# Optimization experiments

Measured on AMD Instinct MI355X. Metric: run time of the kernel, lower is better.

The kernel has to match this reference:

```python
import jax, jax.numpy as jnp
import numpy as np

B, H, W, C = 32, 64, 64, 512
NUM_HEADS = 16
WS = 8          # window_size
SHIFT = 4       # shift_size = WS // 2
MLP_HIDDEN = 2048
N = WS * WS     # tokens per window
NW = (H // WS) * (W // WS)  # windows per image


def _rel_coords_table():
    # Swin-V2 log-spaced continuous relative coordinates, (1, 2*WS-1, 2*WS-1, 2)
    r = np.arange(-(WS - 1), WS, dtype=np.float32)
    t = np.stack(np.meshgrid(r, r, indexing='ij'), axis=-1)[None]
    t = t / (WS - 1) * 8.0
    t = np.sign(t) * np.log2(np.abs(t) + 1.0) / np.log2(8.0)
    return t.astype(np.float32)


def _rel_pos_index():
    coords = np.stack(np.meshgrid(np.arange(WS), np.arange(WS), indexing='ij'))
    cf = coords.reshape(2, -1)
    rel = (cf[:, :, None] - cf[:, None, :]).transpose(1, 2, 0)
    rel[..., 0] += WS - 1
    rel[..., 1] += WS - 1
    rel[..., 0] *= 2 * WS - 1
    return rel.sum(-1)  # (N, N) int


def _attn_mask():
    # shifted-window mask: -100 where tokens come from different image regions
    img = np.zeros((H, W), np.float32)
    cnt = 0
    for hs in (slice(0, -WS), slice(-WS, -SHIFT), slice(-SHIFT, None)):
        for ws_ in (slice(0, -WS), slice(-WS, -SHIFT), slice(-SHIFT, None)):
            img[hs, ws_] = cnt
            cnt += 1
    mw = img.reshape(H // WS, WS, W // WS, WS).transpose(0, 2, 1, 3).reshape(-1, N)
    diff = mw[:, None, :] - mw[:, :, None]
    return np.where(diff != 0, np.float32(-100.0), np.float32(0.0))  # (NW, N, N)


_RCT = jnp.asarray(_rel_coords_table())
_RPI = jnp.asarray(_rel_pos_index().reshape(-1))
_MASK = jnp.asarray(_attn_mask())
_LOGIT_MAX = float(np.log(1.0 / 0.01))


def _layernorm(x, w, b):
    mu = x.mean(-1, keepdims=True)
    var = ((x - mu) ** 2).mean(-1, keepdims=True)
    return (x - mu) / jnp.sqrt(var + 1e-5) * w + b


def setup_inputs() -> dict:
    key = jax.random.key(0)
    ks = jax.random.split(key, 8)
    s = 0.02
    return {
        'x': jax.random.normal(ks[0], (B, H * W, C), jnp.float32),
        'qkv_w': jax.random.normal(ks[1], (3 * C, C), jnp.float32) * s,
        'q_bias': jnp.zeros((C,), jnp.float32),
        'v_bias': jnp.zeros((C,), jnp.float32),
        'logit_scale': jnp.log(10.0 * jnp.ones((NUM_HEADS, 1, 1), jnp.float32)),
        'cpb_w1': jax.random.normal(ks[2], (512, 2), jnp.float32) * s,
        'cpb_b1': jnp.zeros((512,), jnp.float32),
        'cpb_w2': jax.random.normal(ks[3], (NUM_HEADS, 512), jnp.float32) * s,
        'proj_w': jax.random.normal(ks[4], (C, C), jnp.float32) * s,
        'proj_b': jnp.zeros((C,), jnp.float32),
        'norm1_w': jnp.ones((C,), jnp.float32),
        'norm1_b': jnp.zeros((C,), jnp.float32),
        'norm2_w': jnp.ones((C,), jnp.float32),
        'norm2_b': jnp.zeros((C,), jnp.float32),
        'fc1_w': jax.random.normal(ks[5], (MLP_HIDDEN, C), jnp.float32) * s,
        'fc1_b': jnp.zeros((MLP_HIDDEN,), jnp.float32),
        'fc2_w': jax.random.normal(ks[6], (C, MLP_HIDDEN), jnp.float32) * s,
        'fc2_b': jnp.zeros((C,), jnp.float32),
    }


def reference(x, qkv_w, q_bias, v_bias, logit_scale, cpb_w1, cpb_b1, cpb_w2,
              proj_w, proj_b, norm1_w, norm1_b, norm2_w, norm2_b,
              fc1_w, fc1_b, fc2_w, fc2_b):
    hd = C // NUM_HEADS
    shortcut = x
    xi = x.reshape(B, H, W, C)
    xi = jnp.roll(xi, shift=(-SHIFT, -SHIFT), axis=(1, 2))
    # window partition -> (B*NW, N, C)
    xw = xi.reshape(B, H // WS, WS, W // WS, WS, C).transpose(0, 1, 3, 2, 4, 5).reshape(-1, N, C)
    # qkv with q/v bias only (k bias = 0), Swin-V2 style
    qkv_b = jnp.concatenate([q_bias, jnp.zeros_like(v_bias), v_bias])
    qkv = (xw @ qkv_w.T + qkv_b).reshape(-1, N, 3, NUM_HEADS, hd).transpose(2, 0, 3, 1, 4)
    q, k, v = qkv[0], qkv[1], qkv[2]  # (B_, nH, N, hd)
    # cosine attention
    qn = q / jnp.maximum(jnp.linalg.norm(q, axis=-1, keepdims=True), 1e-12)
    kn = k / jnp.maximum(jnp.linalg.norm(k, axis=-1, keepdims=True), 1e-12)
    attn = jnp.einsum('whnd,whmd->whnm', qn, kn)
    scale = jnp.exp(jnp.minimum(logit_scale, _LOGIT_MAX))  # (nH,1,1)
    attn = attn * scale
    # continuous relative position bias via small MLP
    table = (jax.nn.relu(_RCT @ cpb_w1.T + cpb_b1) @ cpb_w2.T).reshape(-1, NUM_HEADS)
    bias = table[_RPI].reshape(N, N, NUM_HEADS).transpose(2, 0, 1)  # (nH, N, N)
    bias = 16.0 * jax.nn.sigmoid(bias)
    attn = attn + bias[None]
    # shift mask
    attn = attn.reshape(B, NW, NUM_HEADS, N, N) + _MASK[None, :, None]
    attn = jax.nn.softmax(attn.reshape(-1, NUM_HEADS, N, N), axis=-1)
    out = jnp.einsum('whnm,whmd->whnd', attn, v).transpose(0, 2, 1, 3).reshape(-1, N, C)
    out = out @ proj_w.T + proj_b
    # window reverse + un-shift
    xi = out.reshape(B, H // WS, W // WS, WS, WS, C).transpose(0, 1, 3, 2, 4, 5).reshape(B, H, W, C)
    xi = jnp.roll(xi, shift=(SHIFT, SHIFT), axis=(1, 2)).reshape(B, H * W, C)
    # Swin-V2 post-norm residuals
    x = shortcut + _layernorm(xi, norm1_w, norm1_b)
    h = jax.nn.gelu(x @ fc1_w.T + fc1_b, approximate=False)
    y = h @ fc2_w.T + fc2_b
    x = x + _layernorm(y, norm2_w, norm2_b)
    return x
```

## Files before the change

kernel.cpp:

```cpp
#include <hip/hip_runtime.h>

typedef unsigned short u16;
typedef unsigned int u32;
typedef __attribute__((ext_vector_type(8))) __bf16 bf16x8;
typedef __attribute__((ext_vector_type(8))) short s16x8;
typedef __attribute__((ext_vector_type(4))) short s16x4;
typedef __attribute__((ext_vector_type(4))) float f32x4;

static __device__ __forceinline__ float bf2f(u16 h){
  union{u32 u; float f;} v; v.u = ((u32)h)<<16; return v.f;
}
static __device__ __forceinline__ u16 cvtbf(float f){
  return __builtin_bit_cast(u16, (__bf16)f);
}

#define GLD16(gp, lp) __builtin_amdgcn_global_load_lds(                      \
  (__attribute__((address_space(1))) void*)(void*)(gp),                      \
  (__attribute__((address_space(3))) void*)(void*)(lp), 16, 0, 0)

__global__ __launch_bounds__(256)
void prep_x_kernel(const float* __restrict__ x, u16* __restrict__ xw)
{
  const int t = threadIdx.x, wv = t>>6, ln = t&63;
  const size_t row = (size_t)blockIdx.x*4 + wv;
  const int b = (int)(row>>12), wl = (int)((row>>6)&63), m = (int)(row&63);
  const int gh = ((wl>>3)*8 + (m>>3) + 4) & 63;
  const int gw = ((wl&7)*8 + (m&7) + 4) & 63;
  const size_t src = ((size_t)b*4096 + (size_t)gh*64 + gw)*512 + (size_t)ln*8;
  f32x4 a = *(const f32x4*)&x[src];
  f32x4 c = *(const f32x4*)&x[src+4];
  s16x8 o;
#pragma unroll
  for (int j=0;j<4;j++){ o[j] = (short)cvtbf(a[j]); o[j+4] = (short)cvtbf(c[j]); }
  *(s16x8*)&xw[row*512 + (size_t)ln*8] = o;
}

__global__ __launch_bounds__(256)
void cvt_bf16_kernel(const float* __restrict__ src, u16* __restrict__ dst, int n)
{
  const int i = (blockIdx.x*256 + threadIdx.x)*8;
  if (i >= n) return;
  f32x4 a = *(const f32x4*)&src[i];
  f32x4 c = *(const f32x4*)&src[i+4];
  s16x8 o;
#pragma unroll
  for (int j=0;j<4;j++){ o[j] = (short)cvtbf(a[j]); o[j+4] = (short)cvtbf(c[j]); }
  *(s16x8*)&dst[i] = o;
}

static __device__ __forceinline__ float logcoord(int d){
  const float tt = (float)d * (8.0f/7.0f);
  const float sg = (tt > 0.f) ? 1.f : ((tt < 0.f) ? -1.f : 0.f);
  return sg * log2f(fabsf(tt) + 1.f) * (1.f/3.f);
}

__global__ __launch_bounds__(512)
void cpb_table_kernel(const float* __restrict__ w1, const float* __restrict__ b1,
                      const float* __restrict__ w2, float* __restrict__ table)
{
  __shared__ float hid[512];
  const int r = blockIdx.x, j = threadIdx.x;
  const float va = logcoord(r/15 - 7);
  const float vb = logcoord(r%15 - 7);
  hid[j] = fmaxf(va*w1[2*j] + vb*w1[2*j+1] + b1[j], 0.f);
  __syncthreads();
  if (j < 16){
    float acc = 0.f;
    for (int i=0;i<512;i++) acc += hid[i]*w2[j*512+i];
    table[r*16 + j] = acc;
  }
}

__global__ __launch_bounds__(256)
void bias_expand_kernel(const float* __restrict__ table, float* __restrict__ biasT)
{
  const int gid = blockIdx.x*256 + threadIdx.x;
  const int h = gid>>12, ij = gid&4095, i = ij>>6, j = ij&63;
  const int dr = (i>>3)-(j>>3)+7, dc = (i&7)-(j&7)+7;
  const float v = table[(dr*15+dc)*16 + h];
  biasT[gid] = 16.f / (1.f + __expf(-v));
}

template<int EPI>
__global__ __launch_bounds__(512)
void gemm256(const u16* __restrict__ A, const u16* __restrict__ B,
             u16* __restrict__ Co, const float* __restrict__ bias0,
             const float* __restrict__ bias1, int N, int K)
{
  extern __shared__ u16 ls[];
  const int t = threadIdx.x;
  const int wv = t>>6, ln = t&63;
  const int wr = wv>>2, wc = wv&3;
  const int lr = ln&15, lg = ln>>4;
  const int gx = gridDim.x;
  const int lin = blockIdx.y*gx + blockIdx.x;
  const int q = (gx*(int)gridDim.y)>>3;
  const int lin2 = (lin&7)*q + (lin>>3);
  const int mT = lin2/gx, nT = lin2 - mT*gx;

  const int rS = wv*32 + (ln>>2);
  const int cS = ((ln&3) ^ ((ln>>3)&3)) * 8;
  const u16* gA0 = A + (size_t)(mT*256 + rS)*K + cS;
  const u16* gB0 = B + (size_t)(nT*256 + rS)*K + cS;
  const size_t rstep = (size_t)16*K;
  char* lW = (char*)ls + wv*2048;

  const int cR = (lg ^ ((lr>>1)&3))*8;
  const int offA0 = (wr*128 + lr)*32 + cR;
  const int offB0 = (wc*64  + lr)*32 + cR;

#define STAGE(buf, tt) do {                                                  \
    char* lb_ = lW + (buf)*32768;                                            \
    const size_t ko_ = (size_t)(tt)*32;                                      \
    GLD16(gA0 + ko_,         lb_);                                           \
    GLD16(gA0 + ko_ + rstep, lb_ + 1024);                                    \
    GLD16(gB0 + ko_,         lb_ + 16384);                                   \
    GLD16(gB0 + ko_ + rstep, lb_ + 16384 + 1024);                            \
  } while(0)

  f32x4 acc[8][4] = {};

#define COMPUTE(buf) do {                                                    \
    const u16* la_ = ls + (buf)*16384;                                       \
    const u16* lb2_ = la_ + 8192;                                            \
    bf16x8 bfr[4];                                                           \
    _Pragma("unroll")                                                        \
    for (int nt=0;nt<4;nt++) bfr[nt] = *(const bf16x8*)&lb2_[offB0 + nt*512];\
    __builtin_amdgcn_s_setprio(1);                                           \
    _Pragma("unroll")                                                        \
    for (int mt=0;mt<8;mt++){                                                \
      bf16x8 af = *(const bf16x8*)&la_[offA0 + mt*512];                      \
      _Pragma("unroll")                                                      \
      for (int nt=0;nt<4;nt++)                                               \
        acc[mt][nt] = __builtin_amdgcn_mfma_f32_16x16x32_bf16(af, bfr[nt], acc[mt][nt], 0,0,0); \
    }                                                                        \
    __builtin_amdgcn_s_setprio(0);                                           \
  } while(0)

  const int nsteps = K>>5;
  STAGE(0,0); STAGE(1,1); STAGE(2,2);
  int cb = 0, sb = 3;
  for (int t_=3; t_<nsteps; ++t_){
    STAGE(sb, t_); sb = (sb==4)?0:sb+1;
    asm volatile("s_waitcnt vmcnt(12)\n\ts_barrier" ::: "memory");
    COMPUTE(cb); cb = (cb==4)?0:cb+1;
  }
  asm volatile("s_waitcnt vmcnt(8)\n\ts_barrier" ::: "memory");
  COMPUTE(cb); cb = (cb==4)?0:cb+1;
  asm volatile("s_waitcnt vmcnt(4)\n\ts_barrier" ::: "memory");
  COMPUTE(cb); cb = (cb==4)?0:cb+1;
  asm volatile("s_waitcnt vmcnt(0)\n\ts_barrier" ::: "memory");
  COMPUTE(cb);
#undef STAGE
#undef COMPUTE

  if (EPI == 0) {
    const int cb0 = nT*256 + wc*64;
    int secA[4], hhA[4], dA[4]; float bbA[4];
#pragma unroll
    for (int nt=0; nt<4; nt++) {
      const int cbp = cb0 + nt*16;
      secA[nt] = cbp >> 9;
      hhA[nt]  = (cbp >> 5) & 15;
      dA[nt]   = (cbp & 16) + lr;
      bbA[nt]  = (secA[nt]==1) ? 0.f : ((secA[nt]==0)?bias0:bias1)[(hhA[nt]<<5)+dA[nt]];
    }
#pragma unroll
    for (int mt=0; mt<8; mt++) {
      const int row = mT*256 + wr*128 + mt*16 + lg*4;
      const int win = row>>6, tok0 = row&63;
#pragma unroll
      for (int rr=0; rr<4; rr++) {
#pragma unroll
        for (int nt=0; nt<4; nt++) {
          u16* p = Co + (size_t)secA[nt]*67108864ULL + (size_t)win*32768
                      + hhA[nt]*2048 + (tok0+rr)*32 + dA[nt];
          *p = cvtbf(acc[mt][nt][rr] + bbA[nt]);
        }
      }
    }
  } else {
    const int c0 = nT*256 + wc*64;
    const int r0 = mT*256 + wr*128 + lg*4;
    float bbA[4];
#pragma unroll
    for (int nt=0; nt<4; nt++) bbA[nt] = bias0[c0 + nt*16 + lr];
#pragma unroll
    for (int mt=0; mt<8; mt++) {
#pragma unroll
      for (int rr=0; rr<4; rr++) {
        u16* pr = Co + (size_t)(r0 + mt*16 + rr)*N + c0 + lr;
#pragma unroll
        for (int nt=0; nt<4; nt++) {
          float v = acc[mt][nt][rr] + bbA[nt];
          if (EPI == 2) {
            const float z = 1.5957691216f * v * fmaf(0.044715f, v*v, 1.0f);
            v = v * __builtin_amdgcn_rcpf(1.0f + __expf(-z));
          }
          pr[nt*16] = cvtbf(v);
        }
      }
    }
  }
}

__global__ __launch_bounds__(256)
void attn_win(const u16* __restrict__ qkv, const float* __restrict__ biasT,
              const float* __restrict__ logit_scale, u16* __restrict__ aout)
{
  __shared__ float sb[4096];
  __shared__ u16 sp[4][4096];
  __shared__ u16 svt[4][2048];
  const int t = threadIdx.x, wv = t>>6, ln = t&63;
  const int lr = ln&15, lg = ln>>4;
  const int head = blockIdx.y;
  for (int i = t; i < 4096; i += 256) sb[i] = biasT[head*4096 + i];
  __syncthreads();
  const int win = blockIdx.x*4 + wv;
  const size_t whi = (size_t)win*16 + head;
  const u16* qb = qkv + whi*2048;
  const u16* kb = qkv + 67108864ULL + whi*2048;
  const u16* vb = qkv + 134217728ULL + whi*2048;

  s16x8 qs[4], ks[4];
  float qin[4], kin[4];
#pragma unroll
  for (int mt=0;mt<4;mt++){
    qs[mt] = *(const s16x8*)&qb[(mt*16+lr)*32 + lg*8];
    float ss = 0.f;
#pragma unroll
    for (int j=0;j<8;j++){ float f = bf2f((u16)qs[mt][j]); ss += f*f; }
    ss += __shfl_xor(ss, 16); ss += __shfl_xor(ss, 32);
    qin[mt] = 1.f / fmaxf(sqrtf(ss), 1e-12f);
  }
#pragma unroll
  for (int nt=0;nt<4;nt++){
    ks[nt] = *(const s16x8*)&kb[(nt*16+lr)*32 + lg*8];
    float ss = 0.f;
#pragma unroll
    for (int j=0;j<8;j++){ float f = bf2f((u16)ks[nt][j]); ss += f*f; }
    ss += __shfl_xor(ss, 16); ss += __shfl_xor(ss, 32);
    kin[nt] = 1.f / fmaxf(sqrtf(ss), 1e-12f);
  }
  f32x4 S[4][4] = {};
#pragma unroll
  for (int mt=0;mt<4;mt++)
#pragma unroll
    for (int nt=0;nt<4;nt++)
      S[mt][nt] = __builtin_amdgcn_mfma_f32_16x16x32_bf16(
          __builtin_bit_cast(bf16x8, qs[mt]), __builtin_bit_cast(bf16x8, ks[nt]),
          S[mt][nt], 0,0,0);

  const float scale = expf(fminf(logit_scale[head], 4.6051702f));
  const int wl = win & 63, wh = wl>>3, ww = wl&7;
  float rsum[4][4];
#pragma unroll
  for (int mt=0;mt<4;mt++){
#pragma unroll
    for (int rr=0;rr<4;rr++){
      const int msub = lg*4 + rr;
      const float qn = __shfl(qin[mt], msub);
      const int m = mt*16 + msub;
      const int ridm = (wh==7 ? (((m>>3)<4) ? 3 : 6) : 0) + (ww==7 ? (((m&7)<4) ? 1 : 2) : 0);
#pragma unroll
      for (int nt=0;nt<4;nt++){
        const int n = nt*16 + lr;
        const int ridn = (wh==7 ? (((n>>3)<4) ? 3 : 6) : 0) + (ww==7 ? (((n&7)<4) ? 1 : 2) : 0);
        float v = S[mt][nt][rr] * (qn * kin[nt] * scale) + sb[m*64+n];
        if (ridm != ridn) v -= 100.f;
        S[mt][nt][rr] = v;
      }
      float mx = fmaxf(fmaxf(S[mt][0][rr], S[mt][1][rr]), fmaxf(S[mt][2][rr], S[mt][3][rr]));
      mx = fmaxf(mx, __shfl_xor(mx, 1)); mx = fmaxf(mx, __shfl_xor(mx, 2));
      mx = fmaxf(mx, __shfl_xor(mx, 4)); mx = fmaxf(mx, __shfl_xor(mx, 8));
      float sm = 0.f;
#pragma unroll
      for (int nt=0;nt<4;nt++){ float p = __expf(S[mt][nt][rr]-mx); S[mt][nt][rr] = p; sm += p; }
      sm += __shfl_xor(sm,1); sm += __shfl_xor(sm,2); sm += __shfl_xor(sm,4); sm += __shfl_xor(sm,8);
      rsum[mt][rr] = sm;
#pragma unroll
      for (int nt=0;nt<4;nt++){
        const int n = nt*16 + lr;
        sp[wv][(m*64 + n) ^ ((m&7)<<3)] = cvtbf(S[mt][nt][rr]);
      }
    }
  }
#pragma unroll
  for (int it=0; it<8; it++){
    const int flat = it*256 + ln*4;
    const int k = flat>>5, d0 = flat&31;
    s16x4 vv = *(const s16x4*)&vb[k*32 + d0];
#pragma unroll
    for (int e=0;e<4;e++)
      svt[wv][((d0+e)*64 + k) ^ (((d0+e)&7)<<3)] = (u16)vv[e];
  }
  f32x4 O[4][2] = {};
#pragma unroll
  for (int kk=0; kk<2; kk++){
    bf16x8 pf[4], vf[2];
#pragma unroll
    for (int mt=0;mt<4;mt++){
      const int am = mt*16 + lr;
      const int idx = (am*64 + kk*32 + lg*8) ^ ((am&7)<<3);
      s16x8 tmp; __builtin_memcpy(&tmp, (const char*)&sp[wv][0] + 2*idx, 16);
      pf[mt] = __builtin_bit_cast(bf16x8, tmp);
    }
#pragma unroll
    for (int n2=0;n2<2;n2++){
      const int vn = n2*16 + lr;
      const int idx = (vn*64 + kk*32 + lg*8) ^ ((vn&7)<<3);
      s16x8 tmp; __builtin_memcpy(&tmp, (const char*)&svt[wv][0] + 2*idx, 16);
      vf[n2] = __builtin_bit_cast(bf16x8, tmp);
    }
#pragma unroll
    for (int mt=0;mt<4;mt++)
#pragma unroll
      for (int n2=0;n2<2;n2++)
        O[mt][n2] = __builtin_amdgcn_mfma_f32_16x16x32_bf16(pf[mt], vf[n2], O[mt][n2], 0,0,0);
  }
  const size_t obase = (size_t)win*64;
#pragma unroll
  for (int mt=0;mt<4;mt++)
#pragma unroll
  for (int rr=0;rr<4;rr++){
    const int m = mt*16 + lg*4 + rr;
    const float inv = 1.f / rsum[mt][rr];
#pragma unroll
    for (int n2=0;n2<2;n2++){
      const int d = n2*16 + lr;
      aout[(obase + m)*512 + head*32 + d] = cvtbf(O[mt][n2][rr] * inv);
    }
  }
}

__global__ __launch_bounds__(256)
void scatter_ln_kernel(const u16* __restrict__ po, const float* __restrict__ x,
                       const float* __restrict__ w, const float* __restrict__ bb,
                       float* __restrict__ x1f, u16* __restrict__ x1b)
{
  const int t = threadIdx.x, wv = t>>6, ln = t&63;
  const size_t row = (size_t)blockIdx.x*4 + wv;
  s16x8 pv = *(const s16x8*)&po[row*512 + (size_t)ln*8];
  float v[8]; float s=0.f, s2=0.f;
#pragma unroll
  for (int j=0;j<8;j++){ v[j] = bf2f((u16)pv[j]); s += v[j]; s2 += v[j]*v[j]; }
#pragma unroll
  for (int d=1; d<64; d<<=1){ s += __shfl_xor(s,d); s2 += __shfl_xor(s2,d); }
  const float mu = s * 0.001953125f;
  const float var = s2 * 0.001953125f - mu*mu;
  const float rs = rsqrtf(var + 1e-5f);
  const int b = (int)(row>>12), wl = (int)((row>>6)&63), m = (int)(row&63);
  const int gh = ((wl>>3)*8 + (m>>3) + 4) & 63;
  const int gw = ((wl&7)*8 + (m&7) + 4) & 63;
  const size_t img = ((size_t)b*4096 + (size_t)gh*64 + gw)*512 + (size_t)ln*8;
  f32x4 xa = *(const f32x4*)&x[img];
  f32x4 xc = *(const f32x4*)&x[img+4];
  f32x4 oa, oc; s16x8 ob;
  const int c0 = ln*8;
#pragma unroll
  for (int j=0;j<8;j++){
    const int c = c0 + j;
    const float lnv = (v[j]-mu)*rs*w[c] + bb[c];
    const float xx = (j<4) ? xa[j] : xc[j-4];
    const float o = xx + lnv;
    if (j<4) oa[j] = o; else oc[j-4] = o;
    ob[j] = (short)cvtbf(o);
  }
  *(f32x4*)&x1f[img] = oa;
  *(f32x4*)&x1f[img+4] = oc;
  *(s16x8*)&x1b[img] = ob;
}

__global__ __launch_bounds__(256)
void final_ln_kernel(const u16* __restrict__ y, const float* __restrict__ w,
                     const float* __restrict__ bb, float* __restrict__ out)
{
  const int t = threadIdx.x, wv = t>>6, ln = t&63;
  const size_t row = (size_t)blockIdx.x*4 + wv;
  s16x8 yv = *(const s16x8*)&y[row*512 + (size_t)ln*8];
  float v[8]; float s=0.f, s2=0.f;
#pragma unroll
  for (int j=0;j<8;j++){ v[j] = bf2f((u16)yv[j]); s += v[j]; s2 += v[j]*v[j]; }
#pragma unroll
  for (int d=1; d<64; d<<=1){ s += __shfl_xor(s,d); s2 += __shfl_xor(s2,d); }
  const float mu = s * 0.001953125f;
  const float var = s2 * 0.001953125f - mu*mu;
  const float rs = rsqrtf(var + 1e-5f);
  const size_t idx = row*512 + (size_t)ln*8;
  f32x4 xa = *(const f32x4*)&out[idx];
  f32x4 xc = *(const f32x4*)&out[idx+4];
  f32x4 oa, oc;
  const int c0 = ln*8;
#pragma unroll
  for (int j=0;j<8;j++){
    const int c = c0 + j;
    const float lnv = (v[j]-mu)*rs*w[c] + bb[c];
    const float xx = (j<4) ? xa[j] : xc[j-4];
    if (j<4) oa[j] = xx + lnv; else oc[j-4] = xx + lnv;
  }
  *(f32x4*)&out[idx] = oa;
  *(f32x4*)&out[idx+4] = oc;
}

extern "C" void kernel_launch(void* const* d_in, const int* in_sizes, int n_in,
                              void* d_out, int out_size, void* d_ws, size_t ws_size,
                              hipStream_t stream)
{
  (void)in_sizes; (void)n_in; (void)out_size; (void)ws_size;
  const float* x        = (const float*)d_in[0];
  const float* qkv_w    = (const float*)d_in[1];
  const float* q_bias   = (const float*)d_in[2];
  const float* v_bias   = (const float*)d_in[3];
  const float* lscale   = (const float*)d_in[4];
  const float* cpb_w1   = (const float*)d_in[5];
  const float* cpb_b1   = (const float*)d_in[6];
  const float* cpb_w2   = (const float*)d_in[7];
  const float* proj_w   = (const float*)d_in[8];
  const float* proj_b   = (const float*)d_in[9];
  const float* n1w      = (const float*)d_in[10];
  const float* n1b      = (const float*)d_in[11];
  const float* n2w      = (const float*)d_in[12];
  const float* n2b      = (const float*)d_in[13];
  const float* fc1_w    = (const float*)d_in[14];
  const float* fc1_b    = (const float*)d_in[15];
  const float* fc2_w    = (const float*)d_in[16];
  const float* fc2_b    = (const float*)d_in[17];

  char* ws = (char*)d_ws;
  constexpr size_t XW_OFF   = 0;
  constexpr size_t ATT_OFF  = 134217728ULL;
  constexpr size_t PRJ_OFF  = 268435456ULL;
  constexpr size_t H_OFF    = 0;
  constexpr size_t BIAS_OFF = 536870912ULL;
  constexpr size_t TAB_OFF  = BIAS_OFF + 262144;
  constexpr size_t WQKV_OFF = TAB_OFF + 16384;
  constexpr size_t WPRJ_OFF = WQKV_OFF + 1572864;
  constexpr size_t WFC1_OFF = WPRJ_OFF + 524288;
  constexpr size_t WFC2_OFF = WFC1_OFF + 2097152;
  constexpr size_t QKV_OFF  = WFC2_OFF + 2097152;
  constexpr size_t X1B_OFF  = QKV_OFF;
  constexpr size_t Y_OFF    = QKV_OFF + 134217728ULL;

  u16*   xw    = (u16*)(ws + XW_OFF);
  u16*   attnO = (u16*)(ws + ATT_OFF);
  u16*   projO = (u16*)(ws + PRJ_OFF);
  u16*   hbuf  = (u16*)(ws + H_OFF);
  float* biasT = (float*)(ws + BIAS_OFF);
  float* table = (float*)(ws + TAB_OFF);
  u16*   wqkv  = (u16*)(ws + WQKV_OFF);
  u16*   wprj  = (u16*)(ws + WPRJ_OFF);
  u16*   wfc1  = (u16*)(ws + WFC1_OFF);
  u16*   wfc2  = (u16*)(ws + WFC2_OFF);
  u16*   qkvB  = (u16*)(ws + QKV_OFF);
  u16*   x1b   = (u16*)(ws + X1B_OFF);
  u16*   ybuf  = (u16*)(ws + Y_OFF);
  float* x1f   = (float*)d_out;

  hipFuncSetAttribute((const void*)gemm256<0>, hipFuncAttributeMaxDynamicSharedMemorySize, 163840);
  hipFuncSetAttribute((const void*)gemm256<1>, hipFuncAttributeMaxDynamicSharedMemorySize, 163840);
  hipFuncSetAttribute((const void*)gemm256<2>, hipFuncAttributeMaxDynamicSharedMemorySize, 163840);
  hipFuncSetAttribute((const void*)gemm256<3>, hipFuncAttributeMaxDynamicSharedMemorySize, 163840);

  cvt_bf16_kernel<<<384, 256, 0, stream>>>(qkv_w, wqkv, 786432);
  cvt_bf16_kernel<<<128, 256, 0, stream>>>(proj_w, wprj, 262144);
  cvt_bf16_kernel<<<512, 256, 0, stream>>>(fc1_w, wfc1, 1048576);
  cvt_bf16_kernel<<<512, 256, 0, stream>>>(fc2_w, wfc2, 1048576);
  prep_x_kernel<<<32768, 256, 0, stream>>>(x, xw);
  cpb_table_kernel<<<225, 512, 0, stream>>>(cpb_w1, cpb_b1, cpb_w2, table);
  bias_expand_kernel<<<256, 256, 0, stream>>>(table, biasT);
  gemm256<0><<<dim3(6,512), 512, 163840, stream>>>(xw, wqkv, qkvB, q_bias, v_bias, 1536, 512);
  attn_win<<<dim3(512,16), 256, 0, stream>>>(qkvB, biasT, lscale, attnO);
  gemm256<1><<<dim3(2,512), 512, 163840, stream>>>(attnO, wprj, projO, proj_b, nullptr, 512, 512);
  scatter_ln_kernel<<<32768, 256, 0, stream>>>(projO, x, n1w, n1b, x1f, x1b);
  gemm256<2><<<dim3(8,512), 512, 163840, stream>>>(x1b, wfc1, hbuf, fc1_b, nullptr, 2048, 512);
  gemm256<3><<<dim3(2,512), 512, 163840, stream>>>(hbuf, wfc2, ybuf, fc2_b, nullptr, 512, 2048);
  final_ln_kernel<<<32768, 256, 0, stream>>>(ybuf, n2w, n2b, (float*)d_out);
}
```

Baseline: 1.650 ms.

## Shrink GEMM tile to 128x256 with triple-buffered pipeline for two blocks per CU

Replaces the 256x256-tile GEMM with a 128x256 tile (4x4 accumulators per wave), a 3-stage LDS ring of 24 KB stages instead of 5 stages of 32 KB, and launch_bounds(512,4). The aim is to cut LDS use from 160 KB to 72 KB and lower register pressure so two blocks fit per CU, letting one block's memory stalls hide behind the other's compute. It also doubles the grid size and drops the setprio hints. In exchange, each block reuses loaded data less (more global traffic per FLOP) and the prefetch depth is shallower.

```diff
diff --git a/kernel.cpp b/kernel.cpp
--- a/kernel.cpp
+++ b/kernel.cpp
@@ -82,8 +82,8 @@
 }
 
 template<int EPI>
-__global__ __launch_bounds__(512)
-void gemm256(const u16* __restrict__ A, const u16* __restrict__ B,
+__global__ __launch_bounds__(512, 4)
+void gemm128(const u16* __restrict__ A, const u16* __restrict__ B,
              u16* __restrict__ Co, const float* __restrict__ bias0,
              const float* __restrict__ bias1, int N, int K)
 {
@@ -98,57 +98,54 @@
   const int lin2 = (lin&7)*q + (lin>>3);
   const int mT = lin2/gx, nT = lin2 - mT*gx;
 
-  const int rS = wv*32 + (ln>>2);
+  const int rSub = ln>>2;
   const int cS = ((ln&3) ^ ((ln>>3)&3)) * 8;
-  const u16* gA0 = A + (size_t)(mT*256 + rS)*K + cS;
-  const u16* gB0 = B + (size_t)(nT*256 + rS)*K + cS;
-  const size_t rstep = (size_t)16*K;
-  char* lW = (char*)ls + wv*2048;
+  const u16* gA = A + (size_t)(mT*128 + wv*16 + rSub)*K + cS;
+  const u16* gB = B + (size_t)(nT*256 + wv*16 + rSub)*K + cS;
+  const size_t rstepB = (size_t)128*K;
+  char* lA = (char*)ls + wv*1024;
 
   const int cR = (lg ^ ((lr>>1)&3))*8;
-  const int offA0 = (wr*128 + lr)*32 + cR;
-  const int offB0 = (wc*64  + lr)*32 + cR;
+  const int offA0 = (wr*64 + lr)*32 + cR;
+  const int offB0 = (wc*64 + lr)*32 + cR;
 
 #define STAGE(buf, tt) do {                                                  \
-    char* lb_ = lW + (buf)*32768;                                            \
+    char* p_ = lA + (buf)*24576;                                             \
     const size_t ko_ = (size_t)(tt)*32;                                      \
-    GLD16(gA0 + ko_,         lb_);                                           \
-    GLD16(gA0 + ko_ + rstep, lb_ + 1024);                                    \
-    GLD16(gB0 + ko_,         lb_ + 16384);                                   \
-    GLD16(gB0 + ko_ + rstep, lb_ + 16384 + 1024);                            \
+    GLD16(gA + ko_,          p_);                                            \
+    GLD16(gB + ko_,          p_ + 8192);                                     \
+    GLD16(gB + ko_ + rstepB, p_ + 16384);                                    \
   } while(0)
 
-  f32x4 acc[8][4] = {};
+  f32x4 acc[4][4] = {};
 
 #define COMPUTE(buf) do {                                                    \
-    const u16* la_ = ls + (buf)*16384;                                       \
-    const u16* lb2_ = la_ + 8192;                                            \
+    const u16* la_ = ls + (buf)*12288;                                       \
+    const u16* lb_ = la_ + 4096;                                             \
     bf16x8 bfr[4];                                                           \
     _Pragma("unroll")                                                        \
-    for (int nt=0;nt<4;nt++) bfr[nt] = *(const bf16x8*)&lb2_[offB0 + nt*512];\
-    __builtin_amdgcn_s_setprio(1);                                           \
+    for (int nt=0;nt<4;nt++) bfr[nt] = *(const bf16x8*)&lb_[offB0 + nt*512]; \
     _Pragma("unroll")                                                        \
-    for (int mt=0;mt<8;mt++){                                                \
+    for (int mt=0;mt<4;mt++){                                                \
       bf16x8 af = *(const bf16x8*)&la_[offA0 + mt*512];                      \
       _Pragma("unroll")                                                      \
       for (int nt=0;nt<4;nt++)                                               \
         acc[mt][nt] = __builtin_amdgcn_mfma_f32_16x16x32_bf16(af, bfr[nt], acc[mt][nt], 0,0,0); \
     }                                                                        \
-    __builtin_amdgcn_s_setprio(0);                                           \
   } while(0)
 
   const int nsteps = K>>5;
-  STAGE(0,0); STAGE(1,1); STAGE(2,2);
-  int cb = 0, sb = 3;
-  for (int t_=3; t_<nsteps; ++t_){
-    STAGE(sb, t_); sb = (sb==4)?0:sb+1;
-    asm volatile("s_waitcnt vmcnt(12)\n\ts_barrier" ::: "memory");
-    COMPUTE(cb); cb = (cb==4)?0:cb+1;
-  }
-  asm volatile("s_waitcnt vmcnt(8)\n\ts_barrier" ::: "memory");
-  COMPUTE(cb); cb = (cb==4)?0:cb+1;
-  asm volatile("s_waitcnt vmcnt(4)\n\ts_barrier" ::: "memory");
-  COMPUTE(cb); cb = (cb==4)?0:cb+1;
+  STAGE(0,0); STAGE(1,1);
+  int cb = 0;
+  for (int t_=0; t_<nsteps-1; ++t_){
+    asm volatile("s_waitcnt vmcnt(3)\n\ts_barrier" ::: "memory");
+    if (t_+2 < nsteps){
+      int sb = cb+2; if (sb>=3) sb-=3;
+      STAGE(sb, t_+2);
+    }
+    COMPUTE(cb);
+    cb = (cb==2)?0:cb+1;
+  }
   asm volatile("s_waitcnt vmcnt(0)\n\ts_barrier" ::: "memory");
   COMPUTE(cb);
 #undef STAGE
@@ -166,8 +163,8 @@
       bbA[nt]  = (secA[nt]==1) ? 0.f : ((secA[nt]==0)?bias0:bias1)[(hhA[nt]<<5)+dA[nt]];
     }
 #pragma unroll
-    for (int mt=0; mt<8; mt++) {
-      const int row = mT*256 + wr*128 + mt*16 + lg*4;
+    for (int mt=0; mt<4; mt++) {
+      const int row = mT*128 + wr*64 + mt*16 + lg*4;
       const int win = row>>6, tok0 = row&63;
 #pragma unroll
       for (int rr=0; rr<4; rr++) {
@@ -181,12 +178,12 @@
     }
   } else {
     const int c0 = nT*256 + wc*64;
-    const int r0 = mT*256 + wr*128 + lg*4;
+    const int r0 = mT*128 + wr*64 + lg*4;
     float bbA[4];
 #pragma unroll
     for (int nt=0; nt<4; nt++) bbA[nt] = bias0[c0 + nt*16 + lr];
 #pragma unroll
-    for (int mt=0; mt<8; mt++) {
+    for (int mt=0; mt<4; mt++) {
 #pragma unroll
       for (int rr=0; rr<4; rr++) {
         u16* pr = Co + (size_t)(r0 + mt*16 + rr)*N + c0 + lr;
@@ -456,10 +453,10 @@
   u16*   ybuf  = (u16*)(ws + Y_OFF);
   float* x1f   = (float*)d_out;
 
-  hipFuncSetAttribute((const void*)gemm256<0>, hipFuncAttributeMaxDynamicSharedMemorySize, 163840);
-  hipFuncSetAttribute((const void*)gemm256<1>, hipFuncAttributeMaxDynamicSharedMemorySize, 163840);
-  hipFuncSetAttribute((const void*)gemm256<2>, hipFuncAttributeMaxDynamicSharedMemorySize, 163840);
-  hipFuncSetAttribute((const void*)gemm256<3>, hipFuncAttributeMaxDynamicSharedMemorySize, 163840);
+  hipFuncSetAttribute((const void*)gemm128<0>, hipFuncAttributeMaxDynamicSharedMemorySize, 73728);
+  hipFuncSetAttribute((const void*)gemm128<1>, hipFuncAttributeMaxDynamicSharedMemorySize, 73728);
+  hipFuncSetAttribute((const void*)gemm128<2>, hipFuncAttributeMaxDynamicSharedMemorySize, 73728);
+  hipFuncSetAttribute((const void*)gemm128<3>, hipFuncAttributeMaxDynamicSharedMemorySize, 73728);
 
   cvt_bf16_kernel<<<384, 256, 0, stream>>>(qkv_w, wqkv, 786432);
   cvt_bf16_kernel<<<128, 256, 0, stream>>>(proj_w, wprj, 262144);
@@ -468,11 +465,11 @@
   prep_x_kernel<<<32768, 256, 0, stream>>>(x, xw);
   cpb_table_kernel<<<225, 512, 0, stream>>>(cpb_w1, cpb_b1, cpb_w2, table);
   bias_expand_kernel<<<256, 256, 0, stream>>>(table, biasT);
-  gemm256<0><<<dim3(6,512), 512, 163840, stream>>>(xw, wqkv, qkvB, q_bias, v_bias, 1536, 512);
+  gemm128<0><<<dim3(6,1024), 512, 73728, stream>>>(xw, wqkv, qkvB, q_bias, v_bias, 1536, 512);
   attn_win<<<dim3(512,16), 256, 0, stream>>>(qkvB, biasT, lscale, attnO);
-  gemm256<1><<<dim3(2,512), 512, 163840, stream>>>(attnO, wprj, projO, proj_b, nullptr, 512, 512);
+  gemm128<1><<<dim3(2,1024), 512, 73728, stream>>>(attnO, wprj, projO, proj_b, nullptr, 512, 512);
   scatter_ln_kernel<<<32768, 256, 0, stream>>>(projO, x, n1w, n1b, x1f, x1b);
-  gemm256<2><<<dim3(8,512), 512, 163840, stream>>>(x1b, wfc1, hbuf, fc1_b, nullptr, 2048, 512);
-  gemm256<3><<<dim3(2,512), 512, 163840, stream>>>(hbuf, wfc2, ybuf, fc2_b, nullptr, 512, 2048);
+  gemm128<2><<<dim3(8,1024), 512, 73728, stream>>>(x1b, wfc1, hbuf, fc1_b, nullptr, 2048, 512);
+  gemm128<3><<<dim3(2,1024), 512, 73728, stream>>>(hbuf, wfc2, ybuf, fc2_b, nullptr, 512, 2048);
   final_ln_kernel<<<32768, 256, 0, stream>>>(ybuf, n2w, n2b, (float*)d_out);
 }
```

After: 1.605 ms. -2.7%, faster.
